# Kernel optimization log

Hardware: AMD Instinct MI355X
Metric: run time of the kernel (lower is better)

The kernel has to match this reference:

```python
import jax, jax.numpy as jnp
import numpy as np

B, T = 8, 512
V, H = 2048, 4
N_EMBD = 768


def setup_inputs() -> dict:
    key = jax.random.key(0)
    k1, k2, k3, k4 = jax.random.split(key, 4)
    x = jax.random.randint(k1, (B, T, 1), 0, V, dtype=jnp.int64)
    cooc = jax.random.normal(k2, (V, V, H), dtype=jnp.float32)
    proj_w = jax.random.normal(k3, (N_EMBD, V * H * H), dtype=jnp.float32) * 0.01
    proj_b = jax.random.normal(k4, (N_EMBD,), dtype=jnp.float32)
    return {"x": x, "cooc": cooc, "proj_w": proj_w, "proj_b": proj_b}


def reference(x, cooc, proj_w, proj_b):
    # x: [B,T,1] int token ids; cooc: [V,V,H]
    tok = x[..., 0]  # [B,T]
    Vv, _, Hh = cooc.shape
    Bb, Tt = tok.shape
    # att scores: wei[b,i,j,h] = cooc[tok[b,i], tok[b,j], h]  (keys index rows, queries cols)
    wei = cooc[tok[:, :, None], tok[:, None, :], :]  # [B,T,T,H]
    att = jax.nn.softmax(wei, axis=2)  # softmax over last token axis (dim=-1 of [T,T])
    att = att + jnp.eye(Tt, dtype=att.dtype)[None, :, :, None]  # self loops
    # value embedding table is flatten(cooc, 1, 2): [V, V*H]; same for every head
    v = cooc.reshape(Vv, Vv * Hh)[tok]  # [B,T,V*H]
    # per-head: att[:,:,:,h] @ v -> [B,T,V*H]; concat over heads on last dim
    out = jnp.einsum('bijh,bjd->bihd', att, v)  # [B,T,H,V*H]
    out = out.reshape(Bb, Tt, Hh * Vv * Hh)  # [B,T,H*V*H]
    # projection (dropout p=0.0 / eval mode -> identity)
    y = out @ proj_w.T + proj_b  # [B,T,n_embd]
    return y
```

## Files before the change

kernel.cpp:

```cpp
#include <hip/hip_runtime.h>
#include <stdint.h>

#define B_    8
#define T_    512
#define V_    2048
#define H_    4
#define NE_   768
#define D_    8192
#define PWROW 32768
#define M1    3072
#define K3    2048
#define MTT_E 6291456UL

#define AS1 __attribute__((address_space(1)))
#define AS3 __attribute__((address_space(3)))

typedef __attribute__((ext_vector_type(8))) short bf16x8;
typedef __attribute__((ext_vector_type(4))) float f32x4;

__device__ __forceinline__ unsigned short f2bf(float f) {
  union { float f; unsigned int u; } c; c.f = f;
  unsigned int u = c.u;
  return (unsigned short)((u + 0x7FFFu + ((u >> 16) & 1u)) >> 16);
}
__device__ __forceinline__ float bf2f(unsigned short s) {
  union { unsigned int u; float f; } c; c.u = ((unsigned int)s) << 16;
  return c.f;
}

__global__ __launch_bounds__(256) void cvtAB_k(
    const float* __restrict__ cooc, const float* __restrict__ pw,
    unsigned short* __restrict__ dst, int bq4, int n4) {
  int i = blockIdx.x * 256 + threadIdx.x;
  const int stride = gridDim.x * 256;
  for (; i < n4; i += stride) {
    const float4 v = (i < bq4) ? ((const float4*)cooc)[i]
                               : ((const float4*)pw)[i - bq4];
    ushort4 o;
    o.x = f2bf(v.x); o.y = f2bf(v.y); o.z = f2bf(v.z); o.w = f2bf(v.w);
    ((ushort4*)dst)[i] = o;
  }
}

__global__ __launch_bounds__(512, 2) void gemm1p_k(
    const unsigned short* __restrict__ Aq,
    const unsigned short* __restrict__ Bq,
    unsigned short* __restrict__ P,
    int kk_per) {
  __shared__ unsigned short lds[2][2][256 * 64];
  const int r0 = blockIdx.x * 256;
  const int t0 = blockIdx.y * 256;
  const int z  = blockIdx.z;
  const int kbeg = z * kk_per;
  const int NT = kk_per / 64;
  const int tid  = threadIdx.x;
  const int lane = tid & 63, w = tid >> 6;
  const int wm = w >> 2, wn = w & 3;
  const int fr = lane & 15, fq = lane >> 4;
  unsigned short* __restrict__ Pz = P + (size_t)z * MTT_E;

  f32x4 acc[8][4];
  #pragma unroll
  for (int m = 0; m < 8; ++m)
    #pragma unroll
    for (int n = 0; n < 4; ++n) acc[m][n] = (f32x4){0.f, 0.f, 0.f, 0.f};

  auto STAGE = [&](int d, int k0) {
    #pragma unroll
    for (int i = 0; i < 4; ++i) {
      const int q   = (w * 4 + i) * 64 + lane;
      const int row = q >> 3;
      const int c16 = (q & 7) ^ (row & 7);
      __builtin_amdgcn_global_load_lds(
          (const AS1 void*)(Aq + (size_t)(r0 + row) * D_ + k0 + c16 * 8),
          (AS3 void*)(&lds[d][0][(w * 4 + i) * 512]), 16, 0, 0);
    }
    #pragma unroll
    for (int i = 0; i < 4; ++i) {
      const int q   = (w * 4 + i) * 64 + lane;
      const int row = q >> 3;
      const int c16 = (q & 7) ^ (row & 7);
      __builtin_amdgcn_global_load_lds(
          (const AS1 void*)(Bq + (size_t)(t0 + row) * D_ + k0 + c16 * 8),
          (AS3 void*)(&lds[d][1][(w * 4 + i) * 512]), 16, 0, 0);
    }
  };
  #define OFFS(r, c) ((r) * 64 + (((c) ^ ((r) & 7)) * 8))

  STAGE(0, kbeg);

  for (int kt = 0; kt < NT; ++kt) {
    if (kt + 1 < NT) {
      STAGE((kt + 1) & 1, kbeg + (kt + 1) * 64);
      asm volatile("s_waitcnt vmcnt(8)" ::: "memory");
    } else {
      asm volatile("s_waitcnt vmcnt(0)" ::: "memory");
    }
    __builtin_amdgcn_s_barrier();
    __builtin_amdgcn_sched_barrier(0);

    const unsigned short* Ab = &lds[kt & 1][0][0];
    const unsigned short* Bb = &lds[kt & 1][1][0];

    bf16x8 afA[4][2], afB[4][2], bf0[2][2], bf1[2][2];
    #pragma unroll
    for (int m = 0; m < 4; ++m)
      #pragma unroll
      for (int kk = 0; kk < 2; ++kk)
        afA[m][kk] = *(const bf16x8*)&Ab[OFFS(wm * 128 + m * 16 + fr, kk * 4 + fq)];
    #pragma unroll
    for (int n = 0; n < 2; ++n)
      #pragma unroll
      for (int kk = 0; kk < 2; ++kk) {
        bf0[n][kk] = *(const bf16x8*)&Bb[OFFS(wn * 64 + n * 16 + fr, kk * 4 + fq)];
        bf1[n][kk] = *(const bf16x8*)&Bb[OFFS(wn * 64 + 32 + n * 16 + fr, kk * 4 + fq)];
      }

    __builtin_amdgcn_s_setprio(1);
    #pragma unroll
    for (int m = 0; m < 4; ++m)
      #pragma unroll
      for (int n = 0; n < 2; ++n)
        #pragma unroll
        for (int kk = 0; kk < 2; ++kk) {
          acc[m][n]     = __builtin_amdgcn_mfma_f32_16x16x32_bf16(afA[m][kk], bf0[n][kk], acc[m][n], 0, 0, 0);
          acc[m][n + 2] = __builtin_amdgcn_mfma_f32_16x16x32_bf16(afA[m][kk], bf1[n][kk], acc[m][n + 2], 0, 0, 0);
        }
    #pragma unroll
    for (int m = 0; m < 4; ++m)
      #pragma unroll
      for (int kk = 0; kk < 2; ++kk)
        afB[m][kk] = *(const bf16x8*)&Ab[OFFS(wm * 128 + 64 + m * 16 + fr, kk * 4 + fq)];
    #pragma unroll
    for (int m = 0; m < 4; ++m)
      #pragma unroll
      for (int n = 0; n < 2; ++n)
        #pragma unroll
        for (int kk = 0; kk < 2; ++kk) {
          acc[m + 4][n]     = __builtin_amdgcn_mfma_f32_16x16x32_bf16(afB[m][kk], bf0[n][kk], acc[m + 4][n], 0, 0, 0);
          acc[m + 4][n + 2] = __builtin_amdgcn_mfma_f32_16x16x32_bf16(afB[m][kk], bf1[n][kk], acc[m + 4][n + 2], 0, 0, 0);
        }
    __builtin_amdgcn_s_setprio(0);

    __builtin_amdgcn_s_barrier();
    __builtin_amdgcn_sched_barrier(0);
  }
  #undef OFFS

  #pragma unroll
  for (int m = 0; m < 8; ++m)
    #pragma unroll
    for (int n = 0; n < 4; ++n) {
      const int rbase = r0 + wm * 128 + m * 16 + fq * 4;
      const int t = t0 + wn * 64 + n * 16 + fr;
      ushort4 o;
      o.x = f2bf(acc[m][n][0]); o.y = f2bf(acc[m][n][1]);
      o.z = f2bf(acc[m][n][2]); o.w = f2bf(acc[m][n][3]);
      *(ushort4*)&Pz[(size_t)(rbase >> 2) * D_ + t * H_] = o;
    }
}

__global__ __launch_bounds__(256) void gemm1f_k(
    const unsigned short* __restrict__ Aq,
    const unsigned short* __restrict__ Bq,
    unsigned short* __restrict__ P, int kk) {
  __shared__ unsigned short As[128 * 32];
  __shared__ unsigned short Bs[128 * 32];
  const int r0 = blockIdx.x * 128;
  const int t0 = blockIdx.y * 128;
  const int z  = blockIdx.z;
  const int kbeg = z * kk, kend = kbeg + kk;
  const int tid  = threadIdx.x;
  const int lane = tid & 63, wave = tid >> 6;
  const int wr = wave >> 1, wc = wave & 1;
  const int fr = lane & 15, fq = lane >> 4;
  const int l4 = lane >> 2, lb = lane & 3;
  unsigned short* __restrict__ Pz = P + (size_t)z * MTT_E;

  f32x4 acc[4][4];
  #pragma unroll
  for (int m = 0; m < 4; ++m)
    #pragma unroll
    for (int n = 0; n < 4; ++n) acc[m][n] = (f32x4){0.f, 0.f, 0.f, 0.f};

  for (int k0 = kbeg; k0 < kend; k0 += 32) {
    __syncthreads();
    #pragma unroll
    for (int c = 0; c < 2; ++c) {
      const int ch  = wave * 2 + c;
      const int row = ch * 16 + l4;
      __builtin_amdgcn_global_load_lds(
          (const AS1 void*)(Aq + (size_t)(r0 + row) * D_ + k0 + lb * 8),
          (AS3 void*)(As + ch * 512), 16, 0, 0);
      __builtin_amdgcn_global_load_lds(
          (const AS1 void*)(Bq + (size_t)(t0 + row) * D_ + k0 + lb * 8),
          (AS3 void*)(Bs + ch * 512), 16, 0, 0);
    }
    __syncthreads();
    bf16x8 af[4], bf[4];
    #pragma unroll
    for (int m = 0; m < 4; ++m)
      af[m] = *(const bf16x8*)&As[(wr * 64 + m * 16 + fr) * 32 + fq * 8];
    #pragma unroll
    for (int n = 0; n < 4; ++n)
      bf[n] = *(const bf16x8*)&Bs[(wc * 64 + n * 16 + fr) * 32 + fq * 8];
    #pragma unroll
    for (int m = 0; m < 4; ++m)
      #pragma unroll
      for (int n = 0; n < 4; ++n)
        acc[m][n] = __builtin_amdgcn_mfma_f32_16x16x32_bf16(af[m], bf[n], acc[m][n], 0, 0, 0);
  }
  #pragma unroll
  for (int m = 0; m < 4; ++m)
    #pragma unroll
    for (int n = 0; n < 4; ++n) {
      const int rbase = r0 + wr * 64 + m * 16 + fq * 4;
      const int t = t0 + wc * 64 + n * 16 + fr;
      ushort4 o;
      o.x = f2bf(acc[m][n][0]); o.y = f2bf(acc[m][n][1]);
      o.z = f2bf(acc[m][n][2]); o.w = f2bf(acc[m][n][3]);
      *(ushort4*)&Pz[(size_t)(rbase >> 2) * D_ + t * H_] = o;
    }
}

__global__ __launch_bounds__(256) void rgather_k(
    const unsigned short* __restrict__ P, const int* __restrict__ x,
    unsigned short* __restrict__ GT, int nz) {
  __shared__ int toks[B_ * T_];
  __shared__ unsigned short row[D_];
  const int tid = threadIdx.x;
  #pragma unroll
  for (int c = 0; c < 16; ++c) toks[c * 256 + tid] = x[c * 256 + tid];

  const int e = blockIdx.x;
  const unsigned short* prow = P + (size_t)e * D_;

  float s[8][4];
  #pragma unroll
  for (int i = 0; i < 8; ++i) { s[i][0] = s[i][1] = s[i][2] = s[i][3] = 0.f; }
  for (int z = 0; z < nz; ++z) {
    const unsigned short* pz = prow + (size_t)z * MTT_E;
    #pragma unroll
    for (int i = 0; i < 8; ++i) {
      const ushort4 v = *(const ushort4*)(pz + (size_t)(i * 256 + tid) * 4);
      s[i][0] += bf2f(v.x); s[i][1] += bf2f(v.y);
      s[i][2] += bf2f(v.z); s[i][3] += bf2f(v.w);
    }
  }
  #pragma unroll
  for (int i = 0; i < 8; ++i) {
    ushort4 o;
    o.x = f2bf(s[i][0]); o.y = f2bf(s[i][1]);
    o.z = f2bf(s[i][2]); o.w = f2bf(s[i][3]);
    *(ushort4*)&row[(i * 256 + tid) * 4] = o;
  }
  __syncthreads();

  const int lane = tid & 63, wave = tid >> 6;
  #pragma unroll
  for (int bb = 0; bb < 2; ++bb) {
    const int b = wave * 2 + bb;
    unsigned short* grow = GT + ((size_t)b * NE_ + e) * K3;
    const int* tb = toks + b * T_;
    #pragma unroll
    for (int r = 0; r < 8; ++r) {
      const int j = r * 64 + lane;
      const uint2 v = *(const uint2*)&row[tb[j] * H_];
      *(uint2*)(grow + j * H_) = v;
    }
  }
}

__global__ __launch_bounds__(256) void gemm3f_k(
    const unsigned short* __restrict__ att,
    const unsigned short* __restrict__ GT,
    const float* __restrict__ bias,
    float* __restrict__ y) {
  __shared__ unsigned short As[128 * 32];
  __shared__ unsigned short Bs[64 * 32];
  const int b  = blockIdx.z;
  const int i0 = blockIdx.x * 128;
  const int e0 = blockIdx.y * 64;
  const int tid  = threadIdx.x;
  const int lane = tid & 63, wave = tid >> 6;
  const int wr = wave >> 1, wc = wave & 1;
  const int fr = lane & 15, fq = lane >> 4;

  f32x4 acc[4][2];
  #pragma unroll
  for (int m = 0; m < 4; ++m)
    #pragma unroll
    for (int n = 0; n < 2; ++n) acc[m][n] = (f32x4){0.f, 0.f, 0.f, 0.f};

  const unsigned short* aB = att + (size_t)(b * T_ + i0) * K3;
  const unsigned short* bB = GT + ((size_t)b * NE_ + e0) * K3;

  for (int k0 = 0; k0 < K3; k0 += 32) {
    __syncthreads();
    #pragma unroll
    for (int rdi = 0; rdi < 2; ++rdi) {
      const int q = rdi * 256 + tid;
      const int row = q >> 2, koff = (q & 3) * 8;
      __builtin_amdgcn_global_load_lds(
          (const AS1 void*)(aB + (size_t)row * K3 + k0 + koff),
          (AS3 void*)(As + q * 8), 16, 0, 0);
    }
    {
      const int q = tid;
      const int row = q >> 2, koff = (q & 3) * 8;
      __builtin_amdgcn_global_load_lds(
          (const AS1 void*)(bB + (size_t)row * K3 + k0 + koff),
          (AS3 void*)(Bs + q * 8), 16, 0, 0);
    }
    __syncthreads();
    bf16x8 af[4], bf[2];
    #pragma unroll
    for (int m = 0; m < 4; ++m)
      af[m] = *(const bf16x8*)&As[(wr * 64 + m * 16 + fr) * 32 + fq * 8];
    #pragma unroll
    for (int n = 0; n < 2; ++n)
      bf[n] = *(const bf16x8*)&Bs[(wc * 32 + n * 16 + fr) * 32 + fq * 8];
    #pragma unroll
    for (int m = 0; m < 4; ++m)
      #pragma unroll
      for (int n = 0; n < 2; ++n)
        acc[m][n] = __builtin_amdgcn_mfma_f32_16x16x32_bf16(af[m], bf[n], acc[m][n], 0, 0, 0);
  }

  #pragma unroll
  for (int m = 0; m < 4; ++m)
    #pragma unroll
    for (int n = 0; n < 2; ++n) {
      const int i = i0 + wr * 64 + m * 16 + fq * 4;
      const int e = e0 + wc * 32 + n * 16 + fr;
      const float be = bias[e];
      #pragma unroll
      for (int g = 0; g < 4; ++g)
        y[(size_t)(b * T_ + i + g) * NE_ + e] = acc[m][n][g] + be;
    }
}

__global__ __launch_bounds__(64) void softmax_k(
    const int* __restrict__ x, const float* __restrict__ cooc,
    unsigned short* __restrict__ att) {
  const int bi = blockIdx.x;
  const int b = bi >> 9, i = bi & (T_ - 1);
  const int lane = threadIdx.x;
  const int ti = x[b * T_ + i];
  const float* crow = cooc + (size_t)ti * D_;

  float w[8][4];
  #pragma unroll
  for (int r = 0; r < 8; ++r) {
    const int j = lane + r * 64;
    const int tj = x[b * T_ + j];
    const float4 v = *(const float4*)(crow + (size_t)tj * H_);
    w[r][0] = v.x; w[r][1] = v.y; w[r][2] = v.z; w[r][3] = v.w;
  }
  float m[4] = {-1e30f, -1e30f, -1e30f, -1e30f};
  #pragma unroll
  for (int r = 0; r < 8; ++r)
    #pragma unroll
    for (int h = 0; h < 4; ++h) m[h] = fmaxf(m[h], w[r][h]);
  #pragma unroll
  for (int off = 32; off > 0; off >>= 1)
    #pragma unroll
    for (int h = 0; h < 4; ++h) m[h] = fmaxf(m[h], __shfl_xor(m[h], off));
  float s[4] = {0.f, 0.f, 0.f, 0.f};
  #pragma unroll
  for (int r = 0; r < 8; ++r)
    #pragma unroll
    for (int h = 0; h < 4; ++h) { w[r][h] = __expf(w[r][h] - m[h]); s[h] += w[r][h]; }
  #pragma unroll
  for (int off = 32; off > 0; off >>= 1)
    #pragma unroll
    for (int h = 0; h < 4; ++h) s[h] += __shfl_xor(s[h], off);
  float inv[4];
  #pragma unroll
  for (int h = 0; h < 4; ++h) inv[h] = 1.f / s[h];

  unsigned short* arow = att + (size_t)(b * T_ + i) * (T_ * H_);
  #pragma unroll
  for (int r = 0; r < 8; ++r) {
    const int j = lane + r * 64;
    const float d = (j == i) ? 1.f : 0.f;
    ushort4 o;
    o.x = f2bf(w[r][0] * inv[0] + d);
    o.y = f2bf(w[r][1] * inv[1] + d);
    o.z = f2bf(w[r][2] * inv[2] + d);
    o.w = f2bf(w[r][3] * inv[3] + d);
    *(ushort4*)(arow + (size_t)j * H_) = o;
  }
}

__global__ __launch_bounds__(256) void gemm1_k(
    const float* __restrict__ pw, const float* __restrict__ cooc,
    unsigned short* __restrict__ mtT) {
  __shared__ unsigned short As[128 * 32];
  __shared__ unsigned short Bs[64 * 32];
  const int h  = blockIdx.z;
  const int e0 = blockIdx.x * 128;
  const int t0 = blockIdx.y * 64;
  const int tid  = threadIdx.x;
  const int lane = tid & 63, wave = tid >> 6;
  const int wr = wave >> 1, wc = wave & 1;
  const int fr = lane & 15, fq = lane >> 4;

  f32x4 acc[4][2];
  #pragma unroll
  for (int m = 0; m < 4; ++m)
    #pragma unroll
    for (int n = 0; n < 2; ++n) acc[m][n] = (f32x4){0.f, 0.f, 0.f, 0.f};

  const float* aB = pw + (size_t)e0 * PWROW + (size_t)h * D_;
  const float* bB = cooc + (size_t)t0 * D_;

  for (int k0 = 0; k0 < D_; k0 += 32) {
    __syncthreads();
    #pragma unroll
    for (int c = 0; c < 4; ++c) {
      const int fe = (c * 256 + tid) * 4;
      const int row = fe >> 5, k = fe & 31;
      const float4 v = *(const float4*)(aB + (size_t)row * PWROW + k0 + k);
      ushort4 o; o.x = f2bf(v.x); o.y = f2bf(v.y); o.z = f2bf(v.z); o.w = f2bf(v.w);
      *(ushort4*)&As[fe] = o;
    }
    #pragma unroll
    for (int c = 0; c < 2; ++c) {
      const int fe = (c * 256 + tid) * 4;
      const int row = fe >> 5, k = fe & 31;
      const float4 v = *(const float4*)(bB + (size_t)row * D_ + k0 + k);
      ushort4 o; o.x = f2bf(v.x); o.y = f2bf(v.y); o.z = f2bf(v.z); o.w = f2bf(v.w);
      *(ushort4*)&Bs[fe] = o;
    }
    __syncthreads();
    bf16x8 af[4], bf[2];
    #pragma unroll
    for (int m = 0; m < 4; ++m)
      af[m] = *(const bf16x8*)&As[(wr * 64 + m * 16 + fr) * 32 + fq * 8];
    #pragma unroll
    for (int n = 0; n < 2; ++n)
      bf[n] = *(const bf16x8*)&Bs[(wc * 32 + n * 16 + fr) * 32 + fq * 8];
    #pragma unroll
    for (int m = 0; m < 4; ++m)
      #pragma unroll
      for (int n = 0; n < 2; ++n)
        acc[m][n] = __builtin_amdgcn_mfma_f32_16x16x32_bf16(af[m], bf[n], acc[m][n], 0, 0, 0);
  }
  #pragma unroll
  for (int m = 0; m < 4; ++m)
    #pragma unroll
    for (int n = 0; n < 2; ++n) {
      const int e = e0 + wr * 64 + m * 16 + fq * 4;
      const int t = t0 + wc * 32 + n * 16 + fr;
      #pragma unroll
      for (int g = 0; g < 4; ++g)
        mtT[(size_t)(e + g) * D_ + t * H_ + h] = f2bf(acc[m][n][g]);
    }
}

__global__ __launch_bounds__(256) void gemm3_k(
    const unsigned short* __restrict__ att, const unsigned short* __restrict__ mtT,
    const int* __restrict__ x, const float* __restrict__ bias,
    float* __restrict__ y) {
  __shared__ unsigned short As[64 * 32];
  __shared__ unsigned short Bs[128 * 32];
  const int b  = blockIdx.z;
  const int i0 = blockIdx.x * 64;
  const int e0 = blockIdx.y * 128;
  const int tid  = threadIdx.x;
  const int lane = tid & 63, wave = tid >> 6;
  const int wr = wave >> 1, wc = wave & 1;
  const int fr = lane & 15, fq = lane >> 4;

  f32x4 acc[2][4];
  #pragma unroll
  for (int m = 0; m < 2; ++m)
    #pragma unroll
    for (int n = 0; n < 4; ++n) acc[m][n] = (f32x4){0.f, 0.f, 0.f, 0.f};

  const unsigned short* aB = att + (size_t)(b * T_ + i0) * (T_ * H_);

  for (int ks = 0; ks < 64; ++ks) {
    const int k0 = ks * 32;
    __syncthreads();
    {
      const int fe = tid * 8;
      const int row = fe >> 5, k = fe & 31;
      const uint4 v = *(const uint4*)(aB + (size_t)row * (T_ * H_) + k0 + k);
      *(uint4*)&As[fe] = v;
    }
    #pragma unroll
    for (int c = 0; c < 4; ++c) {
      const int q = c * 256 + tid;
      const int n = q >> 3, j8 = q & 7;
      const int tj = x[b * T_ + ks * 8 + j8];
      const uint2 v = *(const uint2*)(mtT + (size_t)(e0 + n) * D_ + tj * H_);
      *(uint2*)&Bs[n * 32 + j8 * 4] = v;
    }
    __syncthreads();
    bf16x8 af[2], bf[4];
    #pragma unroll
    for (int m = 0; m < 2; ++m)
      af[m] = *(const bf16x8*)&As[(wr * 32 + m * 16 + fr) * 32 + fq * 8];
    #pragma unroll
    for (int n = 0; n < 4; ++n)
      bf[n] = *(const bf16x8*)&Bs[(wc * 64 + n * 16 + fr) * 32 + fq * 8];
    #pragma unroll
    for (int m = 0; m < 2; ++m)
      #pragma unroll
      for (int n = 0; n < 4; ++n)
        acc[m][n] = __builtin_amdgcn_mfma_f32_16x16x32_bf16(af[m], bf[n], acc[m][n], 0, 0, 0);
  }
  #pragma unroll
  for (int m = 0; m < 2; ++m)
    #pragma unroll
    for (int n = 0; n < 4; ++n) {
      const int i = i0 + wr * 32 + m * 16 + fq * 4;
      const int e = e0 + wc * 64 + n * 16 + fr;
      const float be = bias[e];
      #pragma unroll
      for (int g = 0; g < 4; ++g)
        y[(size_t)(b * T_ + i + g) * NE_ + e] = acc[m][n][g] + be;
    }
}

extern "C" void kernel_launch(void* const* d_in, const int* in_sizes, int n_in,
                              void* d_out, int out_size, void* d_ws, size_t ws_size,
                              hipStream_t stream) {
  const int*   x    = (const int*)d_in[0];
  const float* cooc = (const float*)d_in[1];
  const float* pw   = (const float*)d_in[2];
  const float* pb   = (const float*)d_in[3];
  float* y = (float*)d_out;

  const size_t BQ_E = (size_t)V_ * D_;
  const size_t AQ_E = (size_t)M1 * D_;

  unsigned short* mtT = (unsigned short*)d_ws;
  auto need = [&](int c) { return ((size_t)c * MTT_E + BQ_E + AQ_E) * 2; };

  int nz = 0, pipe = 0;
  if      (ws_size >= need(8)) { nz = 8; pipe = 1; }
  else if (ws_size >= need(4)) { nz = 4; pipe = 1; }
  else if (ws_size >= need(2)) { nz = 2; pipe = 0; }
  else if (ws_size >= need(1)) { nz = 1; pipe = 0; }

  if (nz >= 1) {
    unsigned short* Bq  = mtT + (size_t)nz * MTT_E;
    unsigned short* Aq  = Bq + BQ_E;
    unsigned short* GT  = Bq;
    unsigned short* att = Aq;
    hipLaunchKernelGGL(cvtAB_k, dim3(2048), dim3(256), 0, stream,
                       cooc, pw, Bq, (int)(BQ_E / 4), (int)((BQ_E + AQ_E) / 4));
    if (pipe)
      hipLaunchKernelGGL(gemm1p_k, dim3(M1 / 256, V_ / 256, nz), dim3(512), 0,
                         stream, Aq, Bq, mtT, D_ / nz);
    else
      hipLaunchKernelGGL(gemm1f_k, dim3(M1 / 128, V_ / 128, nz), dim3(256), 0,
                         stream, Aq, Bq, mtT, D_ / nz);
    hipLaunchKernelGGL(softmax_k, dim3(B_ * T_), dim3(64), 0, stream, x, cooc, att);
    hipLaunchKernelGGL(rgather_k, dim3(NE_), dim3(256), 0, stream, mtT, x, GT, nz);
    hipLaunchKernelGGL(gemm3f_k, dim3(T_ / 128, NE_ / 64, B_), dim3(256), 0, stream,
                       att, GT, pb, y);
  } else {
    unsigned short* att = mtT + MTT_E;
    hipLaunchKernelGGL(gemm1_k, dim3(NE_ / 128, V_ / 64, H_), dim3(256), 0, stream,
                       pw, cooc, mtT);
    hipLaunchKernelGGL(softmax_k, dim3(B_ * T_), dim3(64), 0, stream, x, cooc, att);
    hipLaunchKernelGGL(gemm3_k, dim3(T_ / 64, NE_ / 128, B_), dim3(256), 0, stream,
                       att, mtT, x, pb, y);
  }
}
```

Baseline: 229.6 us.

## Fuse proj_w bf16 conversion into GEMM1 A-tile loads via register staging

The projection weight is no longer converted to bf16 in a separate pass. GEMM1 now reads fp32 A tiles straight from global memory into registers, packs them to bf16 and writes them into swizzled LDS, overlapping the next tile's loads with the current MFMA work. This drops the cvt write and re-read of the 3072x8192 A matrix and the non-pipelined fallback GEMM, and reorders rgather before softmax so att can reuse the mtT buffer. In exchange the A operand traffic into GEMM1 doubles to fp32, register pressure goes up, and the pipeline waits on vmcnt(0) each iteration.

Measured after the change: 455.0 us. 98.1% more time.

```diff
diff --git a/kernel.cpp b/kernel.cpp
--- a/kernel.cpp
+++ b/kernel.cpp
@@ -27,23 +27,24 @@
   union { unsigned int u; float f; } c; c.u = ((unsigned int)s) << 16;
   return c.f;
 }
-
-__global__ __launch_bounds__(256) void cvtAB_k(
-    const float* __restrict__ cooc, const float* __restrict__ pw,
-    unsigned short* __restrict__ dst, int bq4, int n4) {
+__device__ __forceinline__ unsigned int pk2(float a, float b) {
+  return (unsigned int)f2bf(a) | ((unsigned int)f2bf(b) << 16);
+}
+
+__global__ __launch_bounds__(256) void cvt_k(
+    const float* __restrict__ src, unsigned short* __restrict__ dst, int n4) {
   int i = blockIdx.x * 256 + threadIdx.x;
   const int stride = gridDim.x * 256;
   for (; i < n4; i += stride) {
-    const float4 v = (i < bq4) ? ((const float4*)cooc)[i]
-                               : ((const float4*)pw)[i - bq4];
+    const float4 v = ((const float4*)src)[i];
     ushort4 o;
     o.x = f2bf(v.x); o.y = f2bf(v.y); o.z = f2bf(v.z); o.w = f2bf(v.w);
     ((ushort4*)dst)[i] = o;
   }
 }
 
-__global__ __launch_bounds__(512, 2) void gemm1p_k(
-    const unsigned short* __restrict__ Aq,
+__global__ __launch_bounds__(512, 2) void gemm1pA_k(
+    const float* __restrict__ A32,
     const unsigned short* __restrict__ Bq,
     unsigned short* __restrict__ P,
     int kk_per) {
@@ -65,16 +66,7 @@
     #pragma unroll
     for (int n = 0; n < 4; ++n) acc[m][n] = (f32x4){0.f, 0.f, 0.f, 0.f};
 
-  auto STAGE = [&](int d, int k0) {
-    #pragma unroll
-    for (int i = 0; i < 4; ++i) {
-      const int q   = (w * 4 + i) * 64 + lane;
-      const int row = q >> 3;
-      const int c16 = (q & 7) ^ (row & 7);
-      __builtin_amdgcn_global_load_lds(
-          (const AS1 void*)(Aq + (size_t)(r0 + row) * D_ + k0 + c16 * 8),
-          (AS3 void*)(&lds[d][0][(w * 4 + i) * 512]), 16, 0, 0);
-    }
+  auto STAGE_B = [&](int d, int k0) {
     #pragma unroll
     for (int i = 0; i < 4; ++i) {
       const int q   = (w * 4 + i) * 64 + lane;
@@ -85,22 +77,51 @@
           (AS3 void*)(&lds[d][1][(w * 4 + i) * 512]), 16, 0, 0);
     }
   };
+  float4 ga[8];
+  auto LOAD_A = [&](int k0) {
+    #pragma unroll
+    for (int i = 0; i < 4; ++i) {
+      const int q = i * 512 + tid;
+      const int row = q >> 3, c = q & 7;
+      const float* src = A32 + (size_t)(r0 + row) * D_ + k0 + c * 8;
+      ga[2 * i]     = *(const float4*)(src);
+      ga[2 * i + 1] = *(const float4*)(src + 4);
+    }
+  };
+  auto WRITE_A = [&](int d) {
+    #pragma unroll
+    for (int i = 0; i < 4; ++i) {
+      const int q = i * 512 + tid;
+      const int row = q >> 3, c = q & 7;
+      const int pc = c ^ (row & 7);
+      int4 o;
+      o.x = (int)pk2(ga[2 * i].x,     ga[2 * i].y);
+      o.y = (int)pk2(ga[2 * i].z,     ga[2 * i].w);
+      o.z = (int)pk2(ga[2 * i + 1].x, ga[2 * i + 1].y);
+      o.w = (int)pk2(ga[2 * i + 1].z, ga[2 * i + 1].w);
+      *(int4*)&lds[d][0][row * 64 + pc * 8] = o;
+    }
+  };
   #define OFFS(r, c) ((r) * 64 + (((c) ^ ((r) & 7)) * 8))
 
-  STAGE(0, kbeg);
+  STAGE_B(0, kbeg);
+  LOAD_A(kbeg);
+  asm volatile("s_waitcnt vmcnt(0)" ::: "memory");
+  WRITE_A(0);
+  asm volatile("s_waitcnt lgkmcnt(0)" ::: "memory");
+  __builtin_amdgcn_sched_barrier(0);
+  __builtin_amdgcn_s_barrier();
+  __builtin_amdgcn_sched_barrier(0);
 
   for (int kt = 0; kt < NT; ++kt) {
-    if (kt + 1 < NT) {
-      STAGE((kt + 1) & 1, kbeg + (kt + 1) * 64);
-      asm volatile("s_waitcnt vmcnt(8)" ::: "memory");
-    } else {
-      asm volatile("s_waitcnt vmcnt(0)" ::: "memory");
-    }
-    __builtin_amdgcn_s_barrier();
-    __builtin_amdgcn_sched_barrier(0);
-
-    const unsigned short* Ab = &lds[kt & 1][0][0];
-    const unsigned short* Bb = &lds[kt & 1][1][0];
+    const int cur = kt & 1, nxt = cur ^ 1;
+    const bool hasnext = (kt + 1 < NT);
+    const int kn = kbeg + (kt + 1) * 64;
+
+    if (hasnext) STAGE_B(nxt, kn);
+
+    const unsigned short* Ab = &lds[cur][0][0];
+    const unsigned short* Bb = &lds[cur][1][0];
 
     bf16x8 afA[4][2], afB[4][2], bf0[2][2], bf1[2][2];
     #pragma unroll
@@ -126,11 +147,17 @@
           acc[m][n]     = __builtin_amdgcn_mfma_f32_16x16x32_bf16(afA[m][kk], bf0[n][kk], acc[m][n], 0, 0, 0);
           acc[m][n + 2] = __builtin_amdgcn_mfma_f32_16x16x32_bf16(afA[m][kk], bf1[n][kk], acc[m][n + 2], 0, 0, 0);
         }
+    __builtin_amdgcn_s_setprio(0);
+
+    if (hasnext) LOAD_A(kn);
+
     #pragma unroll
     for (int m = 0; m < 4; ++m)
       #pragma unroll
       for (int kk = 0; kk < 2; ++kk)
         afB[m][kk] = *(const bf16x8*)&Ab[OFFS(wm * 128 + 64 + m * 16 + fr, kk * 4 + fq)];
+
+    __builtin_amdgcn_s_setprio(1);
     #pragma unroll
     for (int m = 0; m < 4; ++m)
       #pragma unroll
@@ -142,6 +169,12 @@
         }
     __builtin_amdgcn_s_setprio(0);
 
+    if (hasnext) {
+      asm volatile("s_waitcnt vmcnt(0)" ::: "memory");
+      WRITE_A(nxt);
+    }
+    asm volatile("s_waitcnt lgkmcnt(0)" ::: "memory");
+    __builtin_amdgcn_sched_barrier(0);
     __builtin_amdgcn_s_barrier();
     __builtin_amdgcn_sched_barrier(0);
   }
@@ -153,69 +186,6 @@
     for (int n = 0; n < 4; ++n) {
       const int rbase = r0 + wm * 128 + m * 16 + fq * 4;
       const int t = t0 + wn * 64 + n * 16 + fr;
-      ushort4 o;
-      o.x = f2bf(acc[m][n][0]); o.y = f2bf(acc[m][n][1]);
-      o.z = f2bf(acc[m][n][2]); o.w = f2bf(acc[m][n][3]);
-      *(ushort4*)&Pz[(size_t)(rbase >> 2) * D_ + t * H_] = o;
-    }
-}
-
-__global__ __launch_bounds__(256) void gemm1f_k(
-    const unsigned short* __restrict__ Aq,
-    const unsigned short* __restrict__ Bq,
-    unsigned short* __restrict__ P, int kk) {
-  __shared__ unsigned short As[128 * 32];
-  __shared__ unsigned short Bs[128 * 32];
-  const int r0 = blockIdx.x * 128;
-  const int t0 = blockIdx.y * 128;
-  const int z  = blockIdx.z;
-  const int kbeg = z * kk, kend = kbeg + kk;
-  const int tid  = threadIdx.x;
-  const int lane = tid & 63, wave = tid >> 6;
-  const int wr = wave >> 1, wc = wave & 1;
-  const int fr = lane & 15, fq = lane >> 4;
-  const int l4 = lane >> 2, lb = lane & 3;
-  unsigned short* __restrict__ Pz = P + (size_t)z * MTT_E;
-
-  f32x4 acc[4][4];
-  #pragma unroll
-  for (int m = 0; m < 4; ++m)
-    #pragma unroll
-    for (int n = 0; n < 4; ++n) acc[m][n] = (f32x4){0.f, 0.f, 0.f, 0.f};
-
-  for (int k0 = kbeg; k0 < kend; k0 += 32) {
-    __syncthreads();
-    #pragma unroll
-    for (int c = 0; c < 2; ++c) {
-      const int ch  = wave * 2 + c;
-      const int row = ch * 16 + l4;
-      __builtin_amdgcn_global_load_lds(
-          (const AS1 void*)(Aq + (size_t)(r0 + row) * D_ + k0 + lb * 8),
-          (AS3 void*)(As + ch * 512), 16, 0, 0);
-      __builtin_amdgcn_global_load_lds(
-          (const AS1 void*)(Bq + (size_t)(t0 + row) * D_ + k0 + lb * 8),
-          (AS3 void*)(Bs + ch * 512), 16, 0, 0);
-    }
-    __syncthreads();
-    bf16x8 af[4], bf[4];
-    #pragma unroll
-    for (int m = 0; m < 4; ++m)
-      af[m] = *(const bf16x8*)&As[(wr * 64 + m * 16 + fr) * 32 + fq * 8];
-    #pragma unroll
-    for (int n = 0; n < 4; ++n)
-      bf[n] = *(const bf16x8*)&Bs[(wc * 64 + n * 16 + fr) * 32 + fq * 8];
-    #pragma unroll
-    for (int m = 0; m < 4; ++m)
-      #pragma unroll
-      for (int n = 0; n < 4; ++n)
-        acc[m][n] = __builtin_amdgcn_mfma_f32_16x16x32_bf16(af[m], bf[n], acc[m][n], 0, 0, 0);
-  }
-  #pragma unroll
-  for (int m = 0; m < 4; ++m)
-    #pragma unroll
-    for (int n = 0; n < 4; ++n) {
-      const int rbase = r0 + wr * 64 + m * 16 + fq * 4;
-      const int t = t0 + wc * 64 + n * 16 + fr;
       ushort4 o;
       o.x = f2bf(acc[m][n][0]); o.y = f2bf(acc[m][n][1]);
       o.z = f2bf(acc[m][n][2]); o.w = f2bf(acc[m][n][3]);
@@ -535,32 +505,25 @@
   float* y = (float*)d_out;
 
   const size_t BQ_E = (size_t)V_ * D_;
-  const size_t AQ_E = (size_t)M1 * D_;
 
   unsigned short* mtT = (unsigned short*)d_ws;
-  auto need = [&](int c) { return ((size_t)c * MTT_E + BQ_E + AQ_E) * 2; };
-
-  int nz = 0, pipe = 0;
-  if      (ws_size >= need(8)) { nz = 8; pipe = 1; }
-  else if (ws_size >= need(4)) { nz = 4; pipe = 1; }
-  else if (ws_size >= need(2)) { nz = 2; pipe = 0; }
-  else if (ws_size >= need(1)) { nz = 1; pipe = 0; }
-
-  if (nz >= 1) {
+  auto need = [&](int c) { return ((size_t)c * MTT_E + BQ_E) * 2; };
+
+  int nz = 0;
+  if      (ws_size >= need(8)) nz = 8;
+  else if (ws_size >= need(4)) nz = 4;
+  else if (ws_size >= need(2)) nz = 2;
+
+  if (nz >= 2) {
     unsigned short* Bq  = mtT + (size_t)nz * MTT_E;
-    unsigned short* Aq  = Bq + BQ_E;
     unsigned short* GT  = Bq;
-    unsigned short* att = Aq;
-    hipLaunchKernelGGL(cvtAB_k, dim3(2048), dim3(256), 0, stream,
-                       cooc, pw, Bq, (int)(BQ_E / 4), (int)((BQ_E + AQ_E) / 4));
-    if (pipe)
-      hipLaunchKernelGGL(gemm1p_k, dim3(M1 / 256, V_ / 256, nz), dim3(512), 0,
-                         stream, Aq, Bq, mtT, D_ / nz);
-    else
-      hipLaunchKernelGGL(gemm1f_k, dim3(M1 / 128, V_ / 128, nz), dim3(256), 0,
-                         stream, Aq, Bq, mtT, D_ / nz);
+    unsigned short* att = mtT;
+    hipLaunchKernelGGL(cvt_k, dim3(2048), dim3(256), 0, stream,
+                       cooc, Bq, (int)(BQ_E / 4));
+    hipLaunchKernelGGL(gemm1pA_k, dim3(M1 / 256, V_ / 256, nz), dim3(512), 0,
+                       stream, pw, Bq, mtT, D_ / nz);
+    hipLaunchKernelGGL(rgather_k, dim3(NE_), dim3(256), 0, stream, mtT, x, GT, nz);
     hipLaunchKernelGGL(softmax_k, dim3(B_ * T_), dim3(64), 0, stream, x, cooc, att);
-    hipLaunchKernelGGL(rgather_k, dim3(NE_), dim3(256), 0, stream, mtT, x, GT, nz);
     hipLaunchKernelGGL(gemm3f_k, dim3(T_ / 128, NE_ / 64, B_), dim3(256), 0, stream,
                        att, GT, pb, y);
   } else {
```

## Replace 256x256 split-K GEMM with 128x128 tile kernel and fixed split of two

Applied to the files above, without the earlier changes.

Replaces the large 256x256-tile, 512-thread pipelined first GEMM with a 128x128-tile, 256-thread kernel that uses K-steps of 32 and a new LDS swizzle, targeting four blocks per CU. It also caps split-K at two slices instead of up to eight. Fewer slices shrink the partial-product workspace and the reduction traffic in the later gather kernel. The cost is lower operand reuse per tile and more, smaller blocks.

Result: no change. 229.6 us (-0.0%).

```diff
diff --git a/kernel.cpp b/kernel.cpp
--- a/kernel.cpp
+++ b/kernel.cpp
@@ -42,57 +42,53 @@
   }
 }
 
-__global__ __launch_bounds__(512, 2) void gemm1p_k(
+__global__ __launch_bounds__(256, 4) void gemm1r_k(
     const unsigned short* __restrict__ Aq,
     const unsigned short* __restrict__ Bq,
     unsigned short* __restrict__ P,
     int kk_per) {
-  __shared__ unsigned short lds[2][2][256 * 64];
-  const int r0 = blockIdx.x * 256;
-  const int t0 = blockIdx.y * 256;
+  __shared__ unsigned short lds[2][2][128 * 32];
+  const int r0 = blockIdx.x * 128;
+  const int t0 = blockIdx.y * 128;
   const int z  = blockIdx.z;
   const int kbeg = z * kk_per;
-  const int NT = kk_per / 64;
+  const int NT = kk_per / 32;
   const int tid  = threadIdx.x;
   const int lane = tid & 63, w = tid >> 6;
-  const int wm = w >> 2, wn = w & 3;
+  const int wr = w >> 1, wc = w & 1;
   const int fr = lane & 15, fq = lane >> 4;
   unsigned short* __restrict__ Pz = P + (size_t)z * MTT_E;
 
-  f32x4 acc[8][4];
-  #pragma unroll
-  for (int m = 0; m < 8; ++m)
+  f32x4 acc[4][4];
+  #pragma unroll
+  for (int m = 0; m < 4; ++m)
     #pragma unroll
     for (int n = 0; n < 4; ++n) acc[m][n] = (f32x4){0.f, 0.f, 0.f, 0.f};
 
   auto STAGE = [&](int d, int k0) {
     #pragma unroll
-    for (int i = 0; i < 4; ++i) {
-      const int q   = (w * 4 + i) * 64 + lane;
-      const int row = q >> 3;
-      const int c16 = (q & 7) ^ (row & 7);
-      __builtin_amdgcn_global_load_lds(
-          (const AS1 void*)(Aq + (size_t)(r0 + row) * D_ + k0 + c16 * 8),
-          (AS3 void*)(&lds[d][0][(w * 4 + i) * 512]), 16, 0, 0);
-    }
-    #pragma unroll
-    for (int i = 0; i < 4; ++i) {
-      const int q   = (w * 4 + i) * 64 + lane;
-      const int row = q >> 3;
-      const int c16 = (q & 7) ^ (row & 7);
-      __builtin_amdgcn_global_load_lds(
-          (const AS1 void*)(Bq + (size_t)(t0 + row) * D_ + k0 + c16 * 8),
-          (AS3 void*)(&lds[d][1][(w * 4 + i) * 512]), 16, 0, 0);
+    for (int op = 0; op < 2; ++op) {
+      const unsigned short* G = op ? Bq : Aq;
+      const int b0 = op ? t0 : r0;
+      #pragma unroll
+      for (int i = 0; i < 2; ++i) {
+        const int q   = i * 256 + tid;
+        const int row = q >> 2;
+        const int pc  = (q & 3) ^ ((row >> 1) & 3);
+        __builtin_amdgcn_global_load_lds(
+            (const AS1 void*)(G + (size_t)(b0 + row) * D_ + k0 + pc * 8),
+            (AS3 void*)(&lds[d][op][(i * 256 + w * 64) * 8]), 16, 0, 0);
+      }
     }
   };
-  #define OFFS(r, c) ((r) * 64 + (((c) ^ ((r) & 7)) * 8))
+  #define OFFS32(r, c) ((r) * 32 + ((((c) ^ (((r) >> 1) & 3))) * 8))
 
   STAGE(0, kbeg);
 
   for (int kt = 0; kt < NT; ++kt) {
     if (kt + 1 < NT) {
-      STAGE((kt + 1) & 1, kbeg + (kt + 1) * 64);
-      asm volatile("s_waitcnt vmcnt(8)" ::: "memory");
+      STAGE((kt + 1) & 1, kbeg + (kt + 1) * 32);
+      asm volatile("s_waitcnt vmcnt(4)" ::: "memory");
     } else {
       asm volatile("s_waitcnt vmcnt(0)" ::: "memory");
     }
@@ -101,58 +97,33 @@
 
     const unsigned short* Ab = &lds[kt & 1][0][0];
     const unsigned short* Bb = &lds[kt & 1][1][0];
-
-    bf16x8 afA[4][2], afB[4][2], bf0[2][2], bf1[2][2];
-    #pragma unroll
-    for (int m = 0; m < 4; ++m)
-      #pragma unroll
-      for (int kk = 0; kk < 2; ++kk)
-        afA[m][kk] = *(const bf16x8*)&Ab[OFFS(wm * 128 + m * 16 + fr, kk * 4 + fq)];
-    #pragma unroll
-    for (int n = 0; n < 2; ++n)
-      #pragma unroll
-      for (int kk = 0; kk < 2; ++kk) {
-        bf0[n][kk] = *(const bf16x8*)&Bb[OFFS(wn * 64 + n * 16 + fr, kk * 4 + fq)];
-        bf1[n][kk] = *(const bf16x8*)&Bb[OFFS(wn * 64 + 32 + n * 16 + fr, kk * 4 + fq)];
-      }
+    bf16x8 af[4], bf[4];
+    #pragma unroll
+    for (int m = 0; m < 4; ++m)
+      af[m] = *(const bf16x8*)&Ab[OFFS32(wr * 64 + m * 16 + fr, fq)];
+    #pragma unroll
+    for (int n = 0; n < 4; ++n)
+      bf[n] = *(const bf16x8*)&Bb[OFFS32(wc * 64 + n * 16 + fr, fq)];
 
     __builtin_amdgcn_s_setprio(1);
     #pragma unroll
     for (int m = 0; m < 4; ++m)
       #pragma unroll
-      for (int n = 0; n < 2; ++n)
-        #pragma unroll
-        for (int kk = 0; kk < 2; ++kk) {
-          acc[m][n]     = __builtin_amdgcn_mfma_f32_16x16x32_bf16(afA[m][kk], bf0[n][kk], acc[m][n], 0, 0, 0);
-          acc[m][n + 2] = __builtin_amdgcn_mfma_f32_16x16x32_bf16(afA[m][kk], bf1[n][kk], acc[m][n + 2], 0, 0, 0);
-        }
-    #pragma unroll
-    for (int m = 0; m < 4; ++m)
-      #pragma unroll
-      for (int kk = 0; kk < 2; ++kk)
-        afB[m][kk] = *(const bf16x8*)&Ab[OFFS(wm * 128 + 64 + m * 16 + fr, kk * 4 + fq)];
-    #pragma unroll
-    for (int m = 0; m < 4; ++m)
-      #pragma unroll
-      for (int n = 0; n < 2; ++n)
-        #pragma unroll
-        for (int kk = 0; kk < 2; ++kk) {
-          acc[m + 4][n]     = __builtin_amdgcn_mfma_f32_16x16x32_bf16(afB[m][kk], bf0[n][kk], acc[m + 4][n], 0, 0, 0);
-          acc[m + 4][n + 2] = __builtin_amdgcn_mfma_f32_16x16x32_bf16(afB[m][kk], bf1[n][kk], acc[m + 4][n + 2], 0, 0, 0);
-        }
+      for (int n = 0; n < 4; ++n)
+        acc[m][n] = __builtin_amdgcn_mfma_f32_16x16x32_bf16(af[m], bf[n], acc[m][n], 0, 0, 0);
     __builtin_amdgcn_s_setprio(0);
 
     __builtin_amdgcn_s_barrier();
     __builtin_amdgcn_sched_barrier(0);
   }
-  #undef OFFS
-
-  #pragma unroll
-  for (int m = 0; m < 8; ++m)
+  #undef OFFS32
+
+  #pragma unroll
+  for (int m = 0; m < 4; ++m)
     #pragma unroll
     for (int n = 0; n < 4; ++n) {
-      const int rbase = r0 + wm * 128 + m * 16 + fq * 4;
-      const int t = t0 + wn * 64 + n * 16 + fr;
+      const int rbase = r0 + wr * 64 + m * 16 + fq * 4;
+      const int t = t0 + wc * 64 + n * 16 + fr;
       ushort4 o;
       o.x = f2bf(acc[m][n][0]); o.y = f2bf(acc[m][n][1]);
       o.z = f2bf(acc[m][n][2]); o.w = f2bf(acc[m][n][3]);
@@ -540,11 +511,9 @@
   unsigned short* mtT = (unsigned short*)d_ws;
   auto need = [&](int c) { return ((size_t)c * MTT_E + BQ_E + AQ_E) * 2; };
 
-  int nz = 0, pipe = 0;
-  if      (ws_size >= need(8)) { nz = 8; pipe = 1; }
-  else if (ws_size >= need(4)) { nz = 4; pipe = 1; }
-  else if (ws_size >= need(2)) { nz = 2; pipe = 0; }
-  else if (ws_size >= need(1)) { nz = 1; pipe = 0; }
+  int nz = 0;
+  if      (ws_size >= need(2)) nz = 2;
+  else if (ws_size >= need(1)) nz = 1;
 
   if (nz >= 1) {
     unsigned short* Bq  = mtT + (size_t)nz * MTT_E;
@@ -553,12 +522,12 @@
     unsigned short* att = Aq;
     hipLaunchKernelGGL(cvtAB_k, dim3(2048), dim3(256), 0, stream,
                        cooc, pw, Bq, (int)(BQ_E / 4), (int)((BQ_E + AQ_E) / 4));
-    if (pipe)
-      hipLaunchKernelGGL(gemm1p_k, dim3(M1 / 256, V_ / 256, nz), dim3(512), 0,
-                         stream, Aq, Bq, mtT, D_ / nz);
+    if (nz == 2)
+      hipLaunchKernelGGL(gemm1r_k, dim3(M1 / 128, V_ / 128, 2), dim3(256), 0,
+                         stream, Aq, Bq, mtT, D_ / 2);
     else
-      hipLaunchKernelGGL(gemm1f_k, dim3(M1 / 128, V_ / 128, nz), dim3(256), 0,
-                         stream, Aq, Bq, mtT, D_ / nz);
+      hipLaunchKernelGGL(gemm1f_k, dim3(M1 / 128, V_ / 128, 1), dim3(256), 0,
+                         stream, Aq, Bq, mtT, D_);
     hipLaunchKernelGGL(softmax_k, dim3(B_ * T_), dim3(64), 0, stream, x, cooc, att);
     hipLaunchKernelGGL(rgather_k, dim3(NE_), dim3(256), 0, stream, mtT, x, GT, nz);
     hipLaunchKernelGGL(gemm3f_k, dim3(T_ / 128, NE_ / 64, B_), dim3(256), 0, stream,
```

## Add finer-grained pipelined GEMM1 kernel with half-K LDS stages for split-8 path

Applied to the files above, without the earlier changes.

Adds a new gemm1e_k kernel that splits each 64-wide K tile into two 32-wide halves with swizzled LDS layout. It interleaves direct global-to-LDS loads of the next halves with MFMA blocks, using explicit vmcnt waits, sched barriers and s_setprio. The goal is to overlap memory traffic with matrix math more tightly than the previous double-buffered kernel. It is used when the workspace allows the 8-way K split, and adds hand-scheduled complexity with a risk of hazards if the waitcnt accounting is wrong.

Measured after the change: 233.5 us. Within noise of the previous version (+1.7%).

```diff
diff --git a/kernel.cpp b/kernel.cpp
--- a/kernel.cpp
+++ b/kernel.cpp
@@ -27,6 +27,10 @@
   union { unsigned int u; float f; } c; c.u = ((unsigned int)s) << 16;
   return c.f;
 }
+
+#define FENCE_BAR() do { __builtin_amdgcn_sched_barrier(0); \
+                         __builtin_amdgcn_s_barrier(); \
+                         __builtin_amdgcn_sched_barrier(0); } while (0)
 
 __global__ __launch_bounds__(256) void cvtAB_k(
     const float* __restrict__ cooc, const float* __restrict__ pw,
@@ -42,11 +46,145 @@
   }
 }
 
-__global__ __launch_bounds__(512, 2) void gemm1p_k(
+__global__ __launch_bounds__(512, 2) void gemm1e_k(
     const unsigned short* __restrict__ Aq,
     const unsigned short* __restrict__ Bq,
     unsigned short* __restrict__ P,
     int kk_per) {
+  __shared__ unsigned short lds[2][2][2][256 * 32];
+  const int r0 = blockIdx.x * 256;
+  const int t0 = blockIdx.y * 256;
+  const int z  = blockIdx.z;
+  const int kbeg = z * kk_per;
+  const int NT = kk_per / 64;
+  const int tid  = threadIdx.x;
+  const int lane = tid & 63, w = tid >> 6;
+  const int wm = w >> 2, wn = w & 3;
+  const int fr = lane & 15, fq = lane >> 4;
+  unsigned short* __restrict__ Pz = P + (size_t)z * MTT_E;
+
+  f32x4 acc[8][4];
+  #pragma unroll
+  for (int m = 0; m < 8; ++m)
+    #pragma unroll
+    for (int n = 0; n < 4; ++n) acc[m][n] = (f32x4){0.f, 0.f, 0.f, 0.f};
+
+  auto SHALF = [&](int d, int op, int kh, int k0) {
+    const unsigned short* G = op ? Bq : Aq;
+    const int b0 = op ? t0 : r0;
+    #pragma unroll
+    for (int i = 0; i < 2; ++i) {
+      const int ci  = i * 512 + tid;
+      const int row = ci >> 2;
+      const int pc  = (ci & 3) ^ ((row >> 1) & 3);
+      __builtin_amdgcn_global_load_lds(
+          (const AS1 void*)(G + (size_t)(b0 + row) * D_ + k0 + kh * 32 + pc * 8),
+          (AS3 void*)(&lds[d][op][kh][(i * 512 + w * 64) * 8]), 16, 0, 0);
+    }
+  };
+  #define OFS(r, c) ((r) * 32 + ((((c) ^ (((r) >> 1) & 3))) * 8))
+
+  SHALF(0, 0, 0, kbeg); SHALF(0, 1, 0, kbeg);
+  SHALF(0, 0, 1, kbeg); SHALF(0, 1, 1, kbeg);
+  SHALF(1, 0, 0, kbeg + 64); SHALF(1, 1, 0, kbeg + 64);
+  asm volatile("s_waitcnt vmcnt(8)" ::: "memory");
+  FENCE_BAR();
+
+  for (int t = 0; t < NT; ++t) {
+    const int d = t & 1;
+    const int kn1 = kbeg + (t + 1) * 64;
+    const int kn2 = kbeg + (t + 2) * 64;
+    const bool i1 = (t + 1 < NT), i2 = (t + 2 < NT);
+    const bool steady = (t < NT - 2);
+    bf16x8 af[8], bf[2];
+
+    #pragma unroll
+    for (int m = 0; m < 8; ++m)
+      af[m] = *(const bf16x8*)&lds[d][0][0][OFS(wm * 128 + m * 16 + fr, fq)];
+    #pragma unroll
+    for (int n = 0; n < 2; ++n)
+      bf[n] = *(const bf16x8*)&lds[d][1][0][OFS(wn * 64 + n * 16 + fr, fq)];
+    if (i1) SHALF(d ^ 1, 0, 1, kn1);
+    FENCE_BAR();
+    __builtin_amdgcn_s_setprio(1);
+    #pragma unroll
+    for (int m = 0; m < 8; ++m)
+      #pragma unroll
+      for (int n = 0; n < 2; ++n)
+        acc[m][n] = __builtin_amdgcn_mfma_f32_16x16x32_bf16(af[m], bf[n], acc[m][n], 0, 0, 0);
+    __builtin_amdgcn_s_setprio(0);
+    FENCE_BAR();
+
+    #pragma unroll
+    for (int n = 0; n < 2; ++n)
+      bf[n] = *(const bf16x8*)&lds[d][1][0][OFS(wn * 64 + 32 + n * 16 + fr, fq)];
+    if (i1) SHALF(d ^ 1, 1, 1, kn1);
+    FENCE_BAR();
+    __builtin_amdgcn_s_setprio(1);
+    #pragma unroll
+    for (int m = 0; m < 8; ++m)
+      #pragma unroll
+      for (int n = 0; n < 2; ++n)
+        acc[m][n + 2] = __builtin_amdgcn_mfma_f32_16x16x32_bf16(af[m], bf[n], acc[m][n + 2], 0, 0, 0);
+    __builtin_amdgcn_s_setprio(0);
+    if (steady) asm volatile("s_waitcnt vmcnt(8)" ::: "memory");
+    else        asm volatile("s_waitcnt vmcnt(0)" ::: "memory");
+    FENCE_BAR();
+
+    #pragma unroll
+    for (int m = 0; m < 8; ++m)
+      af[m] = *(const bf16x8*)&lds[d][0][1][OFS(wm * 128 + m * 16 + fr, fq)];
+    #pragma unroll
+    for (int n = 0; n < 2; ++n)
+      bf[n] = *(const bf16x8*)&lds[d][1][1][OFS(wn * 64 + 32 + n * 16 + fr, fq)];
+    if (i2) SHALF(d, 0, 0, kn2);
+    FENCE_BAR();
+    __builtin_amdgcn_s_setprio(1);
+    #pragma unroll
+    for (int m = 0; m < 8; ++m)
+      #pragma unroll
+      for (int n = 0; n < 2; ++n)
+        acc[m][n + 2] = __builtin_amdgcn_mfma_f32_16x16x32_bf16(af[m], bf[n], acc[m][n + 2], 0, 0, 0);
+    __builtin_amdgcn_s_setprio(0);
+    FENCE_BAR();
+
+    #pragma unroll
+    for (int n = 0; n < 2; ++n)
+      bf[n] = *(const bf16x8*)&lds[d][1][1][OFS(wn * 64 + n * 16 + fr, fq)];
+    if (i2) SHALF(d, 1, 0, kn2);
+    FENCE_BAR();
+    __builtin_amdgcn_s_setprio(1);
+    #pragma unroll
+    for (int m = 0; m < 8; ++m)
+      #pragma unroll
+      for (int n = 0; n < 2; ++n)
+        acc[m][n] = __builtin_amdgcn_mfma_f32_16x16x32_bf16(af[m], bf[n], acc[m][n], 0, 0, 0);
+    __builtin_amdgcn_s_setprio(0);
+    if (i1) {
+      if (steady) asm volatile("s_waitcnt vmcnt(8)" ::: "memory");
+      else        asm volatile("s_waitcnt vmcnt(0)" ::: "memory");
+    }
+    FENCE_BAR();
+  }
+  #undef OFS
+
+  #pragma unroll
+  for (int m = 0; m < 8; ++m)
+    #pragma unroll
+    for (int n = 0; n < 4; ++n) {
+      const int rbase = r0 + wm * 128 + m * 16 + fq * 4;
+      const int t = t0 + wn * 64 + n * 16 + fr;
+      ushort4 o;
+      o.x = f2bf(acc[m][n][0]); o.y = f2bf(acc[m][n][1]);
+      o.z = f2bf(acc[m][n][2]); o.w = f2bf(acc[m][n][3]);
+      *(ushort4*)&Pz[(size_t)(rbase >> 2) * D_ + t * H_] = o;
+    }
+}
+
+__global__ __launch_bounds__(512, 2) void gemm1p_k(
+    const unsigned short* __restrict__ Aq,
+    const unsigned short* __restrict__ Bq,
+    unsigned short* __restrict__ P, int kk_per) {
   __shared__ unsigned short lds[2][2][256 * 64];
   const int r0 = blockIdx.x * 256;
   const int t0 = blockIdx.y * 256;
@@ -540,11 +678,11 @@
   unsigned short* mtT = (unsigned short*)d_ws;
   auto need = [&](int c) { return ((size_t)c * MTT_E + BQ_E + AQ_E) * 2; };
 
-  int nz = 0, pipe = 0;
-  if      (ws_size >= need(8)) { nz = 8; pipe = 1; }
-  else if (ws_size >= need(4)) { nz = 4; pipe = 1; }
-  else if (ws_size >= need(2)) { nz = 2; pipe = 0; }
-  else if (ws_size >= need(1)) { nz = 1; pipe = 0; }
+  int nz = 0;
+  if      (ws_size >= need(8)) nz = 8;
+  else if (ws_size >= need(4)) nz = 4;
+  else if (ws_size >= need(2)) nz = 2;
+  else if (ws_size >= need(1)) nz = 1;
 
   if (nz >= 1) {
     unsigned short* Bq  = mtT + (size_t)nz * MTT_E;
@@ -553,9 +691,12 @@
     unsigned short* att = Aq;
     hipLaunchKernelGGL(cvtAB_k, dim3(2048), dim3(256), 0, stream,
                        cooc, pw, Bq, (int)(BQ_E / 4), (int)((BQ_E + AQ_E) / 4));
-    if (pipe)
-      hipLaunchKernelGGL(gemm1p_k, dim3(M1 / 256, V_ / 256, nz), dim3(512), 0,
-                         stream, Aq, Bq, mtT, D_ / nz);
+    if (nz == 8)
+      hipLaunchKernelGGL(gemm1e_k, dim3(M1 / 256, V_ / 256, 8), dim3(512), 0,
+                         stream, Aq, Bq, mtT, D_ / 8);
+    else if (nz == 4)
+      hipLaunchKernelGGL(gemm1p_k, dim3(M1 / 256, V_ / 256, 4), dim3(512), 0,
+                         stream, Aq, Bq, mtT, D_ / 4);
     else
       hipLaunchKernelGGL(gemm1f_k, dim3(M1 / 128, V_ / 128, nz), dim3(256), 0,
                          stream, Aq, Bq, mtT, D_ / nz);
```
